# Optimization experiments

Measured on AMD Instinct MI355X. Metric: run time of the kernel, lower is better.

The kernel has to match this reference:

```python
import jax, jax.numpy as jnp
import numpy as np
import math

B, QL, KL, H, QD, KD, VD = 4, 1024, 1024, 16, 1024, 1024, 1024
QH = QD // H  # 64
KH = KD // H  # 64


def setup_inputs() -> dict:
    rng = jax.random.key(0)
    ks = jax.random.split(rng, 8)
    return {
        "query": jax.random.normal(ks[0], (B, QL, QD), jnp.float32),
        "key": jax.random.normal(ks[1], (B, KL, KD), jnp.float32),
        "value": jax.random.normal(ks[2], (B, KL, VD), jnp.float32),
        "pad_mask": jax.random.randint(ks[3], (B, QL), 0, 2),
        "q_w": jax.random.uniform(ks[4], (H, QL, QH), jnp.float32),
        "k_w": jax.random.uniform(ks[5], (H, KL, KH), jnp.float32),
        "v_w": jax.random.uniform(ks[6], (H, KL, KH), jnp.float32),
        "o_w": jax.random.uniform(ks[7], (H * KH, QD), jnp.float32),
    }


def reference(query, key, value, pad_mask, q_w, k_w, v_w, o_w):
    b = query.shape[0]
    h, ql, qh = q_w.shape
    kl, kh = k_w.shape[1], k_w.shape[2]

    # mask construction: causal (triu, offset 1) OR pad mask tiled as in torch repeat+view
    causal = jnp.triu(jnp.ones((ql, kl), jnp.float32), 1) == 1            # [i, j]
    pad = jnp.tile(pad_mask, (1, kl)).reshape(b, ql, kl) == 1             # [b, i, j]
    mask = causal[None, :, :] | pad                                      # [b, i, j]

    # positional per-head projections: free index of input feature dim is summed out
    wq = jnp.einsum('biq,his->bhis', query, q_w)                          # [b, h, i, s]
    wk = jnp.einsum('bjk,hjt->bhjt', key, k_w)                            # [b, h, j, t]
    wv = jnp.einsum('bjv,hjt->bhjt', value, v_w)                          # [b, h, j, t]

    scale = math.sqrt(h)  # torch uses query.size()[1] == head_num after projection
    scores = jnp.einsum('bhis,bhjs->bhij', wq, wk) / scale                # [b, h, i, j]
    scores = jnp.where(mask[:, None, :, :], -jnp.inf, scores)
    scores = jnp.nan_to_num(scores)  # -inf -> finfo.min, matching torch.nan_to_num

    weight = jax.nn.softmax(scores, axis=0)  # unusual: softmax over the batch axis
    heads = jnp.einsum('bhij,bhjt->bhit', weight, wv)                     # [b, h, i, t]
    heads = heads.reshape(b, -1, h * kh)  # torch .view: reinterprets [h,i,t] as [i, h*t]
    return jnp.einsum('bit,to->bio', heads, o_w)                          # [b, i, q_dim]
```

## Files before the change

### kernel.cpp

```cpp
#include <hip/hip_runtime.h>
#include <hip/hip_bf16.h>

#define NB 4
#define NL 1024
#define NH 16
#define ND 1024
#define HD 64
#define FMIN_F32 (-3.4028234663852886e38f)
#define LOG2E 1.4426950408889634f

typedef __bf16 bf16x8 __attribute__((ext_vector_type(8)));
typedef float f32x4 __attribute__((ext_vector_type(4)));
typedef unsigned int u32;

static __device__ inline unsigned short f2bf(float f) {
    __hip_bfloat16 h = __float2bfloat16(f);
    return __builtin_bit_cast(unsigned short, h);
}

static __device__ __forceinline__ u32 cvtpk(float a, float b) {
    u32 r;
    asm("v_cvt_pk_bf16_f32 %0, %1, %2" : "=v"(r) : "v"(a), "v"(b));
    return r;
}

static __device__ __forceinline__ void bfsplit2(float x, float y, u32& hiPk, u32& loPk) {
    hiPk = cvtpk(x, y);
    float hx = __builtin_bit_cast(float, hiPk << 16);
    float hy = __builtin_bit_cast(float, hiPk & 0xffff0000u);
    loPk = cvtpk(x - hx, y - hy);
}

static __device__ __forceinline__ void gload16(void* lds, const void* g) {
    __builtin_amdgcn_global_load_lds(
        (const __attribute__((address_space(1))) u32*)g,
        (__attribute__((address_space(3))) u32*)lds, 16, 0, 0);
}

__global__ __launch_bounds__(256)
void rowsum_kernel(const float* __restrict__ q, const float* __restrict__ k,
                   const float* __restrict__ v, float* __restrict__ out) {
    int gw   = blockIdx.x * 4 + (threadIdx.x >> 6);
    int lane = threadIdx.x & 63;
    int tensor = gw >> 12;
    int row    = gw & 4095;
    const float* src = tensor == 0 ? q : (tensor == 1 ? k : v);
    const float* p = src + (size_t)row * ND;
    float s = 0.f;
#pragma unroll
    for (int t = 0; t < 4; ++t) {
        float4 x = *reinterpret_cast<const float4*>(p + t * 256 + lane * 4);
        s += (x.x + x.y) + (x.z + x.w);
    }
#pragma unroll
    for (int off = 32; off; off >>= 1) s += __shfl_xor(s, off);
    if (lane == 0) out[tensor * (NB * NL) + row] = s;
}

__global__ __launch_bounds__(256)
void prep_kernel(const float* __restrict__ k_w, const float* __restrict__ v_w,
                 const float* __restrict__ o_w, const float* __restrict__ sums,
                 const int* __restrict__ pad,
                 unsigned short* __restrict__ kPhi, unsigned short* __restrict__ kPlo,
                 unsigned short* __restrict__ vP, unsigned short* __restrict__ BP,
                 float* __restrict__ S, float* __restrict__ ksm,
                 float* __restrict__ vsm, float* __restrict__ bsm) {
    __shared__ float tile[64][132];
    __shared__ float vsL[256];
    const int tid = threadIdx.x;
    const int bx  = blockIdx.x;
    const float* ksum = sums + NB * NL;
    const float* vsum = sums + 2 * NB * NL;
    if (bx < 256) {
        const int h = bx >> 4, jt = bx & 15;
        char* hiT = (char*)kPhi + (size_t)(h * 16 + jt) * 8192;
        char* loT = (char*)kPlo + (size_t)(h * 16 + jt) * 8192;
        const int row = tid >> 2;
        const int s0  = (tid & 3) * 16;
        const float* src = k_w + ((size_t)(h * NL + jt * 64 + row)) * HD + s0;
#pragma unroll
        for (int t = 0; t < 4; ++t) {
            float4 x = reinterpret_cast<const float4*>(src)[t];
            u32 h01, l01, h23, l23;
            bfsplit2(x.x, x.y, h01, l01);
            bfsplit2(x.z, x.w, h23, l23);
            int off = (row * 128 + (s0 + 4 * t) * 2) ^ ((row & 7) << 4);
            *(uint2*)(hiT + off) = make_uint2(h01, h23);
            *(uint2*)(loT + off) = make_uint2(l01, l23);
        }
    } else if (bx < 512) {
        const int h = (bx - 256) >> 4, jt = (bx - 256) & 15;
#pragma unroll
        for (int t = 0; t < 4; ++t) {
            int id = tid + 256 * t;
            int j = id >> 4, t4 = (id & 15) * 4;
            *(float4*)&tile[j][t4] =
                *(const float4*)(v_w + ((size_t)(h * NL + jt * 64 + j)) * HD + t4);
        }
        vsL[tid] = vsum[(tid >> 6) * NL + jt * 64 + (tid & 63)];
        __syncthreads();
        char* vT_ = (char*)vP + (size_t)(h * 16 + jt) * 8192;
        const int trow = tid >> 2;
        const int jq   = (tid & 3) * 16;
#pragma unroll
        for (int q = 0; q < 4; ++q) {
            int j4 = jq + 4 * q;
            uint2 u;
            u.x = cvtpk(tile[j4 + 0][trow], tile[j4 + 1][trow]);
            u.y = cvtpk(tile[j4 + 2][trow], tile[j4 + 3][trow]);
            int off = (trow * 128 + j4 * 2) ^ ((trow & 7) << 4);
            *(uint2*)(vT_ + off) = u;
        }
        if (jt >= 1) {
            const int b = tid >> 6, t = tid & 63;
            float a = 0.f;
#pragma unroll 16
            for (int j = 0; j < 64; ++j)
                a = fmaf(vsL[b * 64 + j], tile[j][t], a);
            S[(((size_t)h * 16 + jt) * 4 + b) * 64 + t] = a;
        }
    } else if (bx < 640) {
        const int bxo = bx - 512;
        const int ot = bxo >> 4, kt = bxo & 15;
#pragma unroll
        for (int t = 0; t < 8; ++t) {
            int id = tid + 256 * t;
            int c = id >> 5, o4 = (id & 31) * 4;
            *(float4*)&tile[c][o4] =
                *(const float4*)(o_w + ((size_t)(kt * 64 + c)) * ND + ot * 128 + o4);
        }
        __syncthreads();
        char* bT = (char*)BP + (size_t)(ot * 16 + kt) * 16384;
#pragma unroll
        for (int t = 0; t < 8; ++t) {
            int id = tid + 256 * t;
            int ol = id >> 4, c4 = (id & 15) * 4;
            uint2 u;
            u.x = cvtpk(tile[c4 + 0][ol], tile[c4 + 1][ol]);
            u.y = cvtpk(tile[c4 + 2][ol], tile[c4 + 3][ol]);
            int off = (ol * 128 + c4 * 2) ^ ((ol & 7) << 4);
            *(uint2*)(bT + off) = u;
        }
    } else {
        const int e = (bx - 640) * 256 + tid;
        const int j = e >> 2, b = e & 3;
        const int pm = pad[b * NL + j];
        ksm[e] = pm ? 0.f : ksum[b * NL + j] * (LOG2E * 0.25f);
        vsm[e] = vsum[b * NL + j];
        bsm[e] = pm ? FMIN_F32 : 0.f;
    }
}

__global__ __launch_bounds__(512, 4)
void attn_kernel(const float* __restrict__ q_w, const float* __restrict__ sums,
                 const unsigned short* __restrict__ kPhi,
                 const unsigned short* __restrict__ kPlo,
                 const unsigned short* __restrict__ vP,
                 const float* __restrict__ ksm, const float* __restrict__ vsm,
                 const float* __restrict__ bsm, const float* __restrict__ S,
                 unsigned short* __restrict__ AP) {
    __shared__ __align__(16) unsigned short kHi[2][4096], kLo[2][4096], vTl[2][4096];
    __shared__ __align__(16) unsigned short qHi[2048], qLo[2048];
    __shared__ __align__(16) unsigned short wlds[8192];
    __shared__ __align__(16) float qs4[128];
    __shared__ __align__(16) float ks4[2][256];
    __shared__ __align__(16) float vs4[2][256];
    __shared__ __align__(16) float bs4[2][256];

    const float* qsum = sums;

    const int wid = blockIdx.x;
    const int gq  = wid >> 4;
    const int h   = wid & 15;
    const int itp = (gq < 16) ? (2 * gq) : (63 - 2 * gq);
    const int it0 = itp * 32;
    const int cut = (it0 >> 6) + 1;

    const int tid  = threadIdx.x;
    const int lane = tid & 63;
    const int w    = tid >> 6;
    const int l15  = lane & 15;
    const int kb   = (lane >> 4) * 16;

    {
        int row = tid >> 4;
        int s4  = (tid & 15) * 4;
        float4 x = *(const float4*)(q_w + ((size_t)(h * NL + it0 + row)) * HD + s4);
        u32 h01, l01, h23, l23;
        bfsplit2(x.x, x.y, h01, l01);
        bfsplit2(x.z, x.w, h23, l23);
        int off = (row * 128 + s4 * 2) ^ ((row & 7) << 4);
        *(uint2*)((char*)qHi + off) = make_uint2(h01, h23);
        *(uint2*)((char*)qLo + off) = make_uint2(l01, l23);
    }
    if (tid < 128) {
        int b = tid >> 5, i = tid & 31;
        qs4[i * 4 + b] = qsum[b * NL + it0 + i];
    }

    auto stage = [&](int buf, int jt) {
        const size_t tb = (size_t)(h * 16 + jt) * 8192 + tid * 16;
        gload16((char*)kHi[buf] + tid * 16, (const char*)kPhi + tb);
        gload16((char*)kLo[buf] + tid * 16, (const char*)kPlo + tb);
        gload16((char*)vTl[buf] + tid * 16, (const char*)vP + tb);
        if (w == 0)
            gload16((char*)ks4[buf] + lane * 16, (const char*)(ksm + jt * 256) + lane * 16);
        else if (w == 1)
            gload16((char*)vs4[buf] + lane * 16, (const char*)(vsm + jt * 256) + lane * 16);
        else if (w == 2)
            gload16((char*)bs4[buf] + lane * 16, (const char*)(bsm + jt * 256) + lane * 16);
    };

    const int gmi = (w & 1) * 16;
    const int gnj = (w >> 1) * 16;
    const int pb  = w >> 1;
    const int pmh = (w & 1) * 16;

    f32x4 accP[4];
#pragma unroll
    for (int n = 0; n < 4; ++n) accP[n] = (f32x4){0.f, 0.f, 0.f, 0.f};

    stage(0, 0);
    __syncthreads();
    int cur = 0;

    const int i_sm  = gmi + l15;
    const int ig    = it0 + i_sm;
    const int jb_sm = gnj + (lane >> 4) * 4;
    const float4 qsv = *(const float4*)&qs4[i_sm * 4];
    const int woff = (i_sm * 128 + jb_sm * 2) ^ ((i_sm & 7) << 4);

    for (int jt = 0; jt < cut; ++jt) {
        const int j0 = jt * 64;
        if (jt + 1 < cut) stage(cur ^ 1, jt + 1);

        f32x4 gA = (f32x4){0.f, 0.f, 0.f, 0.f};
        f32x4 gB = (f32x4){0.f, 0.f, 0.f, 0.f};
#pragma unroll
        for (int ks = 0; ks < 2; ++ks) {
            const int arow = gnj + l15;
            const int brow = gmi + l15;
            const int aoff = (arow * 128 + ks * 64 + kb) ^ ((arow & 7) << 4);
            const int boff = (brow * 128 + ks * 64 + kb) ^ ((brow & 7) << 4);
            bf16x8 kHiF = __builtin_bit_cast(bf16x8, *(const uint4*)((const char*)kHi[cur] + aoff));
            bf16x8 kLoF = __builtin_bit_cast(bf16x8, *(const uint4*)((const char*)kLo[cur] + aoff));
            bf16x8 qHiF = __builtin_bit_cast(bf16x8, *(const uint4*)((const char*)qHi + boff));
            bf16x8 qLoF = __builtin_bit_cast(bf16x8, *(const uint4*)((const char*)qLo + boff));
            gA = __builtin_amdgcn_mfma_f32_16x16x32_bf16(kHiF, qHiF, gA, 0, 0, 0);
            gA = __builtin_amdgcn_mfma_f32_16x16x32_bf16(kLoF, qHiF, gA, 0, 0, 0);
            gB = __builtin_amdgcn_mfma_f32_16x16x32_bf16(kHiF, qLoF, gB, 0, 0, 0);
        }
        const f32x4 g = gA + gB;

        {
            float wv[4][4];
#pragma unroll
            for (int r = 0; r < 4; ++r) {
                const int j  = jb_sm + r;
                const int jg = j0 + j;
                const float4 ksv = *(const float4*)&ks4[cur][j * 4];
                const float4 vsv = *(const float4*)&vs4[cur][j * 4];
                const float4 bsv = *(const float4*)&bs4[cur][j * 4];
                const float gr = g[r];
                const bool causal = jg > ig;
                float sb0 = fmaf(qsv.x * ksv.x, gr, bsv.x);
                float sb1 = fmaf(qsv.y * ksv.y, gr, bsv.y);
                float sb2 = fmaf(qsv.z * ksv.z, gr, bsv.z);
                float sb3 = fmaf(qsv.w * ksv.w, gr, bsv.w);
                sb0 = causal ? 0.f : sb0;
                sb1 = causal ? 0.f : sb1;
                sb2 = causal ? 0.f : sb2;
                sb3 = causal ? 0.f : sb3;
                const float mx = fmaxf(fmaxf(sb0, sb1), fmaxf(sb2, sb3));
                const float e0 = __builtin_amdgcn_exp2f(sb0 - mx);
                const float e1 = __builtin_amdgcn_exp2f(sb1 - mx);
                const float e2 = __builtin_amdgcn_exp2f(sb2 - mx);
                const float e3 = __builtin_amdgcn_exp2f(sb3 - mx);
                const float inv = __builtin_amdgcn_rcpf((e0 + e1) + (e2 + e3));
                wv[r][0] = e0 * inv * vsv.x;
                wv[r][1] = e1 * inv * vsv.y;
                wv[r][2] = e2 * inv * vsv.z;
                wv[r][3] = e3 * inv * vsv.w;
            }
#pragma unroll
            for (int b = 0; b < 4; ++b) {
                uint2 p;
                p.x = cvtpk(wv[0][b], wv[1][b]);
                p.y = cvtpk(wv[2][b], wv[3][b]);
                *(uint2*)((char*)wlds + b * 4096 + woff) = p;
            }
        }
        asm volatile("s_waitcnt lgkmcnt(0)" ::: "memory");
        __builtin_amdgcn_s_barrier();
        __builtin_amdgcn_sched_barrier(0);

        __builtin_amdgcn_s_setprio(1);
#pragma unroll
        for (int ks = 0; ks < 2; ++ks) {
            const int arow = pmh + l15;
            const int aoff = pb * 4096 + ((arow * 128 + ks * 64 + kb) ^ ((arow & 7) << 4));
            bf16x8 aF = __builtin_bit_cast(bf16x8, *(const uint4*)((const char*)wlds + aoff));
#pragma unroll
            for (int n = 0; n < 4; ++n) {
                const int vrow = n * 16 + l15;
                const int voff = (vrow * 128 + ks * 64 + kb) ^ ((vrow & 7) << 4);
                bf16x8 bF = __builtin_bit_cast(bf16x8, *(const uint4*)((const char*)vTl[cur] + voff));
                accP[n] = __builtin_amdgcn_mfma_f32_16x16x32_bf16(aF, bF, accP[n], 0, 0, 0);
            }
        }
        __builtin_amdgcn_s_setprio(0);
        __syncthreads();
        cur ^= 1;
    }

    if (cut < 16) {
        float sv[4] = {0.f, 0.f, 0.f, 0.f};
        for (int jt = cut; jt < 16; ++jt) {
            const float* sp = S + (((size_t)h * 16 + jt) * 4 + pb) * 64;
#pragma unroll
            for (int n = 0; n < 4; ++n) sv[n] += sp[n * 16 + l15];
        }
#pragma unroll
        for (int n = 0; n < 4; ++n) {
            const float s4v = 0.25f * sv[n];
#pragma unroll
            for (int r = 0; r < 4; ++r) accP[n][r] += s4v;
        }
    }

    {
        const int ib = (it0 + pmh) >> 4;
        char* tbase = (char*)AP + (size_t)((pb * 16 + h) * 16) * 8192;
#pragma unroll
        for (int n = 0; n < 4; ++n)
#pragma unroll
            for (int r = 0; r < 4; ++r) {
                int kt = (lane >> 4) * 4 + r;
                int tt = n * 16 + l15;
                int off = (ib * 128 + tt * 2) ^ ((ib & 7) << 4);
                *(unsigned short*)(tbase + (size_t)kt * 8192 + off) = f2bf(accP[n][r]);
            }
    }
}

__global__ __launch_bounds__(256, 2)
void outgemm_kernel(const unsigned short* __restrict__ AP,
                    const unsigned short* __restrict__ BP,
                    float* __restrict__ out) {
    __shared__ __align__(16) unsigned short aL[3][4096];
    __shared__ __align__(16) unsigned short bL[3][8192];
    const int ox = blockIdx.x;
    const int my = blockIdx.y;
    const int tid  = threadIdx.x;
    const int lane = tid & 63;
    const int w    = tid >> 6;
    const int wr = (w & 1) * 32;
    const int wc = (w >> 1) * 64;
    const int l15  = lane & 15;
    const int kseg = (lane >> 4) * 16;

    f32x4 acc[2][4];
#pragma unroll
    for (int m = 0; m < 2; ++m)
#pragma unroll
        for (int n = 0; n < 4; ++n) acc[m][n] = (f32x4){0.f, 0.f, 0.f, 0.f};

    auto stage = [&](int buf, int kt) {
        const char* at = (const char*)AP + (size_t)(my * 16 + kt) * 8192;
        const char* bt = (const char*)BP + (size_t)(ox * 16 + kt) * 16384;
        gload16((char*)aL[buf] + tid * 16, at + tid * 16);
        gload16((char*)aL[buf] + 4096 + tid * 16, at + 4096 + tid * 16);
#pragma unroll
        for (int r = 0; r < 4; ++r)
            gload16((char*)bL[buf] + r * 4096 + tid * 16, bt + r * 4096 + tid * 16);
    };

    auto compute = [&](int cb) {
        __builtin_amdgcn_s_setprio(1);
#pragma unroll
        for (int ks = 0; ks < 2; ++ks) {
            bf16x8 aF[2], bF[4];
#pragma unroll
            for (int m = 0; m < 2; ++m) {
                int row = wr + m * 16 + l15;
                int off = (row * 128 + ks * 64 + kseg) ^ ((row & 7) << 4);
                aF[m] = __builtin_bit_cast(bf16x8, *(const uint4*)((const char*)aL[cb] + off));
            }
#pragma unroll
            for (int n = 0; n < 4; ++n) {
                int row = wc + n * 16 + l15;
                int off = (row * 128 + ks * 64 + kseg) ^ ((row & 7) << 4);
                bF[n] = __builtin_bit_cast(bf16x8, *(const uint4*)((const char*)bL[cb] + off));
            }
#pragma unroll
            for (int m = 0; m < 2; ++m)
#pragma unroll
                for (int n = 0; n < 4; ++n)
                    acc[m][n] = __builtin_amdgcn_mfma_f32_16x16x32_bf16(
                        aF[m], bF[n], acc[m][n], 0, 0, 0);
        }
        __builtin_amdgcn_s_setprio(0);
    };

    stage(0, 0);
    stage(1, 1);
    for (int kt = 0; kt < 15; ++kt) {
        asm volatile("s_waitcnt vmcnt(6)" ::: "memory");
        __builtin_amdgcn_s_barrier();
        __builtin_amdgcn_sched_barrier(0);
        if (kt + 2 < 16) stage((kt + 2) % 3, kt + 2);
        compute(kt % 3);
    }
    asm volatile("s_waitcnt vmcnt(0)" ::: "memory");
    __builtin_amdgcn_s_barrier();
    __builtin_amdgcn_sched_barrier(0);
    compute(15 % 3);

#pragma unroll
    for (int m = 0; m < 2; ++m)
#pragma unroll
        for (int n = 0; n < 4; ++n)
#pragma unroll
            for (int r = 0; r < 4; ++r) {
                int row = my * 64 + wr + m * 16 + (lane >> 4) * 4 + r;
                int col = ox * 128 + wc + n * 16 + l15;
                out[(size_t)row * ND + col] = acc[m][n][r];
            }
}

extern "C" void kernel_launch(void* const* d_in, const int* in_sizes, int n_in,
                              void* d_out, int out_size, void* d_ws, size_t ws_size,
                              hipStream_t stream) {
    const float* query = (const float*)d_in[0];
    const float* key   = (const float*)d_in[1];
    const float* value = (const float*)d_in[2];
    const int*   pad   = (const int*)d_in[3];
    const float* q_w   = (const float*)d_in[4];
    const float* k_w   = (const float*)d_in[5];
    const float* v_w   = (const float*)d_in[6];
    const float* o_w   = (const float*)d_in[7];
    float* out = (float*)d_out;

    char* W = (char*)d_ws;
    float*          sums = (float*)W;
    unsigned short* kPhi = (unsigned short*)(W + 49152);
    unsigned short* kPlo = (unsigned short*)(W + 2146304);
    unsigned short* vP   = (unsigned short*)(W + 4243456);
    unsigned short* BP   = (unsigned short*)(W + 6340608);
    unsigned short* AP   = (unsigned short*)(W + 8437760);
    float*          ksm  = (float*)(W + 16826368);
    float*          vsm  = (float*)(W + 16842752);
    float*          bsm  = (float*)(W + 16859136);

    float* S = out;

    rowsum_kernel<<<3 * (NB * NL) / 4, 256, 0, stream>>>(query, key, value, sums);

    prep_kernel<<<656, 256, 0, stream>>>(k_w, v_w, o_w, sums, pad,
                                         kPhi, kPlo, vP, BP, S, ksm, vsm, bsm);

    attn_kernel<<<512, 512, 0, stream>>>(q_w, sums, kPhi, kPlo, vP,
                                         ksm, vsm, bsm, S, AP);

    dim3 gg(8, 64);
    outgemm_kernel<<<gg, 256, 0, stream>>>(AP, BP, out);
}
```

Before: 63.15 us.

## Merge rowsum with sum-independent weight prep and split sum-dependent work out

Restructures the preprocessing stages so the row sums and the weight conversions that do not depend on them (K split, V transpose, O_w packing) run together in one launch. The sum-dependent pieces (the S partial products and the ksm/vsm/bsm vectors) move into a small second kernel. This lets the independent conversion work overlap with the rowsum memory traffic instead of waiting behind it. The cost is that v_w tiles are now loaded twice, and the large mixed grid has block types with uneven work.

```diff
diff --git a/kernel.cpp b/kernel.cpp
--- a/kernel.cpp
+++ b/kernel.cpp
@@ -38,41 +38,35 @@
 }
 
 __global__ __launch_bounds__(256)
-void rowsum_kernel(const float* __restrict__ q, const float* __restrict__ k,
-                   const float* __restrict__ v, float* __restrict__ out) {
-    int gw   = blockIdx.x * 4 + (threadIdx.x >> 6);
-    int lane = threadIdx.x & 63;
-    int tensor = gw >> 12;
-    int row    = gw & 4095;
-    const float* src = tensor == 0 ? q : (tensor == 1 ? k : v);
-    const float* p = src + (size_t)row * ND;
-    float s = 0.f;
-#pragma unroll
-    for (int t = 0; t < 4; ++t) {
-        float4 x = *reinterpret_cast<const float4*>(p + t * 256 + lane * 4);
-        s += (x.x + x.y) + (x.z + x.w);
-    }
-#pragma unroll
-    for (int off = 32; off; off >>= 1) s += __shfl_xor(s, off);
-    if (lane == 0) out[tensor * (NB * NL) + row] = s;
-}
-
-__global__ __launch_bounds__(256)
-void prep_kernel(const float* __restrict__ k_w, const float* __restrict__ v_w,
-                 const float* __restrict__ o_w, const float* __restrict__ sums,
-                 const int* __restrict__ pad,
-                 unsigned short* __restrict__ kPhi, unsigned short* __restrict__ kPlo,
-                 unsigned short* __restrict__ vP, unsigned short* __restrict__ BP,
-                 float* __restrict__ S, float* __restrict__ ksm,
-                 float* __restrict__ vsm, float* __restrict__ bsm) {
+void prep1_kernel(const float* __restrict__ query, const float* __restrict__ key,
+                  const float* __restrict__ value,
+                  const float* __restrict__ k_w, const float* __restrict__ v_w,
+                  const float* __restrict__ o_w,
+                  float* __restrict__ sums,
+                  unsigned short* __restrict__ kPhi, unsigned short* __restrict__ kPlo,
+                  unsigned short* __restrict__ vP, unsigned short* __restrict__ BP) {
     __shared__ float tile[64][132];
-    __shared__ float vsL[256];
     const int tid = threadIdx.x;
     const int bx  = blockIdx.x;
-    const float* ksum = sums + NB * NL;
-    const float* vsum = sums + 2 * NB * NL;
-    if (bx < 256) {
-        const int h = bx >> 4, jt = bx & 15;
+    if (bx < 3072) {
+        int gw   = bx * 4 + (tid >> 6);
+        int lane = tid & 63;
+        int tensor = gw >> 12;
+        int row    = gw & 4095;
+        const float* src = tensor == 0 ? query : (tensor == 1 ? key : value);
+        const float* p = src + (size_t)row * ND;
+        float s = 0.f;
+#pragma unroll
+        for (int t = 0; t < 4; ++t) {
+            float4 x = *reinterpret_cast<const float4*>(p + t * 256 + lane * 4);
+            s += (x.x + x.y) + (x.z + x.w);
+        }
+#pragma unroll
+        for (int off = 32; off; off >>= 1) s += __shfl_xor(s, off);
+        if (lane == 0) sums[tensor * (NB * NL) + row] = s;
+    } else if (bx < 3328) {
+        const int idx = bx - 3072;
+        const int h = idx >> 4, jt = idx & 15;
         char* hiT = (char*)kPhi + (size_t)(h * 16 + jt) * 8192;
         char* loT = (char*)kPlo + (size_t)(h * 16 + jt) * 8192;
         const int row = tid >> 2;
@@ -88,8 +82,9 @@
             *(uint2*)(hiT + off) = make_uint2(h01, h23);
             *(uint2*)(loT + off) = make_uint2(l01, l23);
         }
-    } else if (bx < 512) {
-        const int h = (bx - 256) >> 4, jt = (bx - 256) & 15;
+    } else if (bx < 3584) {
+        const int idx = bx - 3328;
+        const int h = idx >> 4, jt = idx & 15;
 #pragma unroll
         for (int t = 0; t < 4; ++t) {
             int id = tid + 256 * t;
@@ -97,30 +92,21 @@
             *(float4*)&tile[j][t4] =
                 *(const float4*)(v_w + ((size_t)(h * NL + jt * 64 + j)) * HD + t4);
         }
-        vsL[tid] = vsum[(tid >> 6) * NL + jt * 64 + (tid & 63)];
         __syncthreads();
         char* vT_ = (char*)vP + (size_t)(h * 16 + jt) * 8192;
         const int trow = tid >> 2;
         const int jq   = (tid & 3) * 16;
 #pragma unroll
-        for (int q = 0; q < 4; ++q) {
-            int j4 = jq + 4 * q;
+        for (int q2 = 0; q2 < 4; ++q2) {
+            int j4 = jq + 4 * q2;
             uint2 u;
             u.x = cvtpk(tile[j4 + 0][trow], tile[j4 + 1][trow]);
             u.y = cvtpk(tile[j4 + 2][trow], tile[j4 + 3][trow]);
             int off = (trow * 128 + j4 * 2) ^ ((trow & 7) << 4);
             *(uint2*)(vT_ + off) = u;
         }
-        if (jt >= 1) {
-            const int b = tid >> 6, t = tid & 63;
-            float a = 0.f;
-#pragma unroll 16
-            for (int j = 0; j < 64; ++j)
-                a = fmaf(vsL[b * 64 + j], tile[j][t], a);
-            S[(((size_t)h * 16 + jt) * 4 + b) * 64 + t] = a;
-        }
-    } else if (bx < 640) {
-        const int bxo = bx - 512;
+    } else {
+        const int bxo = bx - 3584;
         const int ot = bxo >> 4, kt = bxo & 15;
 #pragma unroll
         for (int t = 0; t < 8; ++t) {
@@ -141,8 +127,40 @@
             int off = (ol * 128 + c4 * 2) ^ ((ol & 7) << 4);
             *(uint2*)(bT + off) = u;
         }
+    }
+}
+
+__global__ __launch_bounds__(256)
+void prep2_kernel(const float* __restrict__ v_w, const float* __restrict__ sums,
+                  const int* __restrict__ pad, float* __restrict__ S,
+                  float* __restrict__ ksm, float* __restrict__ vsm,
+                  float* __restrict__ bsm) {
+    __shared__ float tile[64][68];
+    __shared__ float vsL[256];
+    const int tid = threadIdx.x;
+    const int bx  = blockIdx.x;
+    const float* ksum = sums + NB * NL;
+    const float* vsum = sums + 2 * NB * NL;
+    if (bx < 256) {
+        const int h = bx >> 4, jt = bx & 15;
+        if (jt == 0) return;
+#pragma unroll
+        for (int t = 0; t < 4; ++t) {
+            int id = tid + 256 * t;
+            int j = id >> 4, t4 = (id & 15) * 4;
+            *(float4*)&tile[j][t4] =
+                *(const float4*)(v_w + ((size_t)(h * NL + jt * 64 + j)) * HD + t4);
+        }
+        vsL[tid] = vsum[(tid >> 6) * NL + jt * 64 + (tid & 63)];
+        __syncthreads();
+        const int b = tid >> 6, t = tid & 63;
+        float a = 0.f;
+#pragma unroll 16
+        for (int j = 0; j < 64; ++j)
+            a = fmaf(vsL[b * 64 + j], tile[j][t], a);
+        S[(((size_t)h * 16 + jt) * 4 + b) * 64 + t] = a;
     } else {
-        const int e = (bx - 640) * 256 + tid;
+        const int e = (bx - 256) * 256 + tid;
         const int j = e >> 2, b = e & 3;
         const int pm = pad[b * NL + j];
         ksm[e] = pm ? 0.f : ksum[b * NL + j] * (LOG2E * 0.25f);
@@ -454,10 +472,10 @@
 
     float* S = out;
 
-    rowsum_kernel<<<3 * (NB * NL) / 4, 256, 0, stream>>>(query, key, value, sums);
-
-    prep_kernel<<<656, 256, 0, stream>>>(k_w, v_w, o_w, sums, pad,
-                                         kPhi, kPlo, vP, BP, S, ksm, vsm, bsm);
+    prep1_kernel<<<3712, 256, 0, stream>>>(query, key, value, k_w, v_w, o_w,
+                                           sums, kPhi, kPlo, vP, BP);
+
+    prep2_kernel<<<272, 256, 0, stream>>>(v_w, sums, pad, S, ksm, vsm, bsm);
 
     attn_kernel<<<512, 512, 0, stream>>>(q_w, sums, kPhi, kPlo, vP,
                                          ksm, vsm, bsm, S, AP);
```

New measurement: 64.22 us. About the same (+1.7%).
